# Kernel tuning notes

Hardware: AMD Instinct MI355X
Metric: run time of the kernel (lower is better)

## Reference

```python
import jax, jax.numpy as jnp
import numpy as np

S, D = 4096, 64
DROPOUT_P = 0.1


def setup_inputs() -> dict:
    key = jax.random.key(0)
    k1, k2, k3, k4, k5, k6 = jax.random.split(key, 6)
    return {
        "query": jax.random.normal(k1, (S, D), dtype=jnp.float32),
        "key": jax.random.normal(k2, (S, D), dtype=jnp.float32),
        "value": jax.random.normal(k3, (S, D), dtype=jnp.float32),
        "u_drop": jax.random.uniform(k4, (S, S), dtype=jnp.float32),
        "row_rand": jax.random.uniform(k5, (S, 1), dtype=jnp.float32),
        "x": jax.random.normal(k6, (1,), dtype=jnp.float32),
    }


def reference(query, key, value, u_drop, row_rand, x):
    d = query.shape[-1]
    # torch code divides by scale_factor = d**-0.5, i.e. multiplies by sqrt(d)
    qk = jnp.matmul(query, key.T) * jnp.asarray(d, query.dtype) ** 0.5  # [S,S]
    # dropout with keep prob (1-p), inverted scaling (matches F.dropout)
    keep = (u_drop >= DROPOUT_P).astype(qk.dtype) / (1.0 - DROPOUT_P)
    t = qk * keep  # [S,S]
    # drop_rows_or_cols: random floor mask normalized by its global sum
    r = jnp.floor(t * row_rand)          # [S,S] (row_rand broadcasts over cols)
    t = t * (r / jnp.sum(r))             # [S,S]
    return jnp.matmul(t, value)          # [S,D]
```

## Files before the change

### kernel.cpp

```cpp
#include <hip/hip_runtime.h>


#define S 4096
#define D 64
#define NCHUNK 16
#define JCHUNK (S / NCHUNK)
#define JT 64
#define NTILES (JCHUNK / JT)
#define KSCALE (8.0f / 0.9f)

typedef float f32x4 __attribute__((ext_vector_type(4)));
typedef short s16x8 __attribute__((ext_vector_type(8)));
typedef unsigned short u16x4 __attribute__((ext_vector_type(4)));
typedef int i32x4 __attribute__((ext_vector_type(4)));
typedef const __attribute__((address_space(1))) unsigned g_u32;
typedef __attribute__((address_space(3))) unsigned lds_u32;

__device__ inline unsigned short f2bf(float f) {
    union { float f; unsigned u; } v; v.f = f;
    unsigned r = v.u + 0x7fffu + ((v.u >> 16) & 1u);
    return (unsigned short)(r >> 16);
}

__device__ inline unsigned cvt_pk_bf16(float lo, float hi) {
    unsigned r;
    asm("v_cvt_pk_bf16_f32 %0, %1, %2" : "=v"(r) : "v"(lo), "v"(hi));
    return r;
}

__global__ void prep_all(const float* __restrict__ Kf,
                         const float* __restrict__ V,
                         short* __restrict__ Kbf,
                         short* __restrict__ VTbf,
                         int* __restrict__ sumr) {
    __shared__ short tile[64 * 68];
    const int b   = blockIdx.x;
    const int tid = threadIdx.x;
    if (b == 0 && tid == 0) *sumr = 0;

    if (b < 256) {
        const int k = b * 256 + tid;
        float4 v = ((const float4*)Kf)[k];
        u16x4 o; o[0] = f2bf(v.x * KSCALE); o[1] = f2bf(v.y * KSCALE);
                 o[2] = f2bf(v.z * KSCALE); o[3] = f2bf(v.w * KSCALE);
        ((u16x4*)Kbf)[k] = o;
    } else {
        const int j0 = (b - 256) * 64;
#pragma unroll
        for (int it = 0; it < 4; ++it) {
            const int f4 = tid + it * 256;
            const int row = f4 >> 4, c4 = (f4 & 15) * 4;
            float4 v = *(const float4*)&V[(size_t)(j0 + row) * D + c4];
            tile[(c4 + 0) * 68 + row] = (short)f2bf(v.x);
            tile[(c4 + 1) * 68 + row] = (short)f2bf(v.y);
            tile[(c4 + 2) * 68 + row] = (short)f2bf(v.z);
            tile[(c4 + 3) * 68 + row] = (short)f2bf(v.w);
        }
        __syncthreads();
#pragma unroll
        for (int it = 0; it < 4; ++it) {
            const int f4 = tid + it * 256;
            const int d = f4 >> 4, o4 = (f4 & 15) * 4;
            u16x4 w = *(const u16x4*)&tile[d * 68 + o4];
            *(u16x4*)&VTbf[(size_t)d * S + j0 + o4] = w;
        }
    }
}

__launch_bounds__(256, 4)
__global__ void fused_main(const float* __restrict__ Qf,
                           const short* __restrict__ Kbf,
                           const short* __restrict__ VTbf,
                           const float* __restrict__ Ud,
                           const float* __restrict__ RR,
                           float* __restrict__ Opart,
                           int* __restrict__ sumr)
{
    __shared__ short kb[2][8 * 512];
    __shared__ short vb[2][8 * 512];
    __shared__ int red[4];

    const int tid  = threadIdx.x;
    const int w    = tid >> 6;
    const int lane = tid & 63;
    const int quad = lane >> 4;
    const int n16  = lane & 15;

    const int ib  = blockIdx.x & 63;
    const int ic  = blockIdx.x >> 6;
    const int i0w = ib * 64 + w * 16;
    const int jbase = ic * JCHUNK;

    const float* uln = Ud + (size_t)(i0w + n16) * S + quad * 4;

    s16x8 aQ[2];
#pragma unroll
    for (int ks = 0; ks < 2; ++ks) {
        const float* qp = &Qf[(size_t)(i0w + n16) * D + ks * 32 + quad * 8];
        f32x4 qa = *(const f32x4*)qp;
        f32x4 qb = *(const f32x4*)(qp + 4);
        i32x4 aw;
        aw[0] = (int)cvt_pk_bf16(qa[0], qa[1]);
        aw[1] = (int)cvt_pk_bf16(qa[2], qa[3]);
        aw[2] = (int)cvt_pk_bf16(qb[0], qb[1]);
        aw[3] = (int)cvt_pk_bf16(qb[2], qb[3]);
        __builtin_memcpy(&aQ[ks], &aw, 16);
    }

    const float rrn = RR[i0w + n16];

    f32x4 accO[4];
#pragma unroll
    for (int ds = 0; ds < 4; ++ds) accO[ds] = (f32x4){0.f, 0.f, 0.f, 0.f};

    float lsum = 0.f;
    float4 un[4];
    unsigned um;

    {
#pragma unroll
        for (int p = 0; p < 2; ++p) {
            const int e = w * 2 + p;
            __builtin_amdgcn_global_load_lds(
                (g_u32*)&Kbf[(size_t)(jbase + (e >> 1) * 16 + n16) * D + (e & 1) * 32 + quad * 8],
                (lds_u32*)&kb[0][e * 512], 16, 0, 0);
        }
#pragma unroll
        for (int p = 0; p < 2; ++p) {
            const int e = w * 2 + p;
            __builtin_amdgcn_global_load_lds(
                (g_u32*)&VTbf[(size_t)((e & 3) * 16 + n16) * S + jbase + (e >> 2) * 32 + quad * 8],
                (lds_u32*)&vb[0][e * 512], 16, 0, 0);
        }
#pragma unroll
        for (int c = 0; c < 4; ++c)
            un[c] = *(const float4*)&uln[jbase + c * 16];
        __asm__ volatile("s_waitcnt vmcnt(4)" ::: "memory");
        __builtin_amdgcn_s_barrier();
        __asm__ volatile("" ::: "memory");
    }

#pragma unroll
    for (int jt = 0; jt < NTILES; ++jt) {
        const int bu = jt & 1;
        const int nb = bu ^ 1;
        const bool last = (jt + 1 == NTILES);

        if (!last) {
            const int j1 = jbase + (jt + 1) * JT;
#pragma unroll
            for (int p = 0; p < 2; ++p) {
                const int e = w * 2 + p;
                __builtin_amdgcn_global_load_lds(
                    (g_u32*)&Kbf[(size_t)(j1 + (e >> 1) * 16 + n16) * D + (e & 1) * 32 + quad * 8],
                    (lds_u32*)&kb[nb][e * 512], 16, 0, 0);
            }
#pragma unroll
            for (int p = 0; p < 2; ++p) {
                const int e = w * 2 + p;
                __builtin_amdgcn_global_load_lds(
                    (g_u32*)&VTbf[(size_t)((e & 3) * 16 + n16) * S + j1 + (e >> 2) * 32 + quad * 8],
                    (lds_u32*)&vb[nb][e * 512], 16, 0, 0);
            }
        }

        {
            unsigned m = 0;
#pragma unroll
            for (int c = 0; c < 4; ++c) {
                m |= (un[c].x >= 0.1f ? 1u : 0u) << (c * 4 + 0);
                m |= (un[c].y >= 0.1f ? 1u : 0u) << (c * 4 + 1);
                m |= (un[c].z >= 0.1f ? 1u : 0u) << (c * 4 + 2);
                m |= (un[c].w >= 0.1f ? 1u : 0u) << (c * 4 + 3);
            }
            um = m;
        }
        if (!last) {
            const int j1 = jbase + (jt + 1) * JT;
#pragma unroll
            for (int c = 0; c < 4; ++c)
                un[c] = *(const float4*)&uln[j1 + c * 16];
        }

        unsigned pkw[8];
#pragma unroll
        for (int cs = 0; cs < 4; ++cs) {
            f32x4 acc = (f32x4){0.f, 0.f, 0.f, 0.f};
#pragma unroll
            for (int ks = 0; ks < 2; ++ks) {
                s16x8 bK = *(const s16x8*)&kb[bu][(cs * 2 + ks) * 512 + lane * 8];
                acc = __builtin_amdgcn_mfma_f32_16x16x32_bf16(bK, aQ[ks], acc, 0, 0, 0);
            }
            float vv[4];
#pragma unroll
            for (int rg = 0; rg < 4; ++rg) {
                const float t = ((um >> (cs * 4 + rg)) & 1u) ? acc[rg] : 0.0f;
                const float r = floorf(t * rrn);
                lsum += r;
                vv[rg] = t * r;
            }
            pkw[cs * 2]     = cvt_pk_bf16(vv[0], vv[1]);
            pkw[cs * 2 + 1] = cvt_pk_bf16(vv[2], vv[3]);
        }

        const int pbase = (32 * ((lane >> 4) & 1) + n16) * 4;
#pragma unroll
        for (int ksj = 0; ksj < 2; ++ksj) {
            i32x4 aw;
#pragma unroll
            for (int widx = 0; widx < 4; ++widx) {
                const int addr = pbase + (widx >> 1) * 64;
                const int lo = __builtin_amdgcn_ds_bpermute(addr, (int)pkw[ksj * 4 + (widx & 1)]);
                const int hi = __builtin_amdgcn_ds_bpermute(addr, (int)pkw[ksj * 4 + 2 + (widx & 1)]);
                aw[widx] = (lane >= 32) ? hi : lo;
            }
            s16x8 aP;
            __builtin_memcpy(&aP, &aw, 16);
#pragma unroll
            for (int ds = 0; ds < 4; ++ds) {
                s16x8 bV = *(const s16x8*)&vb[bu][(ksj * 4 + ds) * 512 + lane * 8];
                accO[ds] = __builtin_amdgcn_mfma_f32_16x16x32_bf16(aP, bV, accO[ds], 0, 0, 0);
            }
        }

        if (!last) {
            __asm__ volatile("s_waitcnt vmcnt(4)" ::: "memory");
            __builtin_amdgcn_s_barrier();
            __asm__ volatile("" ::: "memory");
        }
    }

    float* op = Opart + (size_t)ic * S * D;
#pragma unroll
    for (int ds = 0; ds < 4; ++ds) {
        const int d = ds * 16 + n16;
#pragma unroll
        for (int rg = 0; rg < 4; ++rg) {
            const int i = i0w + quad * 4 + rg;
            op[(size_t)i * D + d] = accO[ds][rg];
        }
    }

    for (int off = 32; off; off >>= 1) lsum += __shfl_down(lsum, off);
    if (lane == 0) red[w] = (int)lsum;
    __syncthreads();
    if (tid == 0) atomicAdd(sumr, red[0] + red[1] + red[2] + red[3]);
}

__global__ void reduce_out(const float* __restrict__ Opart,
                           const int* __restrict__ sumr,
                           float* __restrict__ out) {
    const int idx = blockIdx.x * 256 + threadIdx.x;
    const float invR = 1.0f / (float)(*sumr);
    float sx = 0.f, sy = 0.f, sz = 0.f, sw = 0.f;
#pragma unroll
    for (int c = 0; c < NCHUNK; ++c) {
        const float4 v = ((const float4*)(Opart + (size_t)c * S * D))[idx];
        sx += v.x; sy += v.y; sz += v.z; sw += v.w;
    }
    float4 o; o.x = sx * invR; o.y = sy * invR; o.z = sz * invR; o.w = sw * invR;
    ((float4*)out)[idx] = o;
}

extern "C" void kernel_launch(void* const* d_in, const int* in_sizes, int n_in,
                              void* d_out, int out_size, void* d_ws, size_t ws_size,
                              hipStream_t stream) {
    (void)in_sizes; (void)n_in; (void)out_size; (void)ws_size;
    const float* Q  = (const float*)d_in[0];
    const float* Kf = (const float*)d_in[1];
    const float* V  = (const float*)d_in[2];
    const float* Ud = (const float*)d_in[3];
    const float* RR = (const float*)d_in[4];
    float* out = (float*)d_out;

    char* ws = (char*)d_ws;
    float* Opart = (float*)ws;
    short* Kbf  = (short*)(ws + (16u << 20));
    short* VTbf = (short*)(ws + (16u << 20) + (512u << 10));
    int*   sumr = (int*)  (ws + (16u << 20) + (1024u << 10));

    prep_all<<<dim3(320), dim3(256), 0, stream>>>(Kf, V, Kbf, VTbf, sumr);
    fused_main<<<dim3(64 * NCHUNK), dim3(256), 0, stream>>>(
        Q, Kbf, VTbf, Ud, RR, Opart, sumr);
    reduce_out<<<dim3(256), dim3(256), 0, stream>>>(Opart, sumr, out);
}
```

Before: 126.2 us.

## Split key dimension into more chunks and drop per-block tile loop

Doubles the number of key-dimension chunks so that each block handles one 128-column tile, loaded in a single shot. This replaces the previous 4-iteration double-buffered loop. The aim is to raise grid parallelism and cut the per-tile barrier and prefetch overhead. In exchange, the partial-output buffer doubles in size, which adds global writes in the main kernel and reads in the reduction kernel. The workspace layout is shifted to make room for it.

Result: slower. 133.0 us (+5.4%).

```diff
diff --git a/kernel.cpp b/kernel.cpp
--- a/kernel.cpp
+++ b/kernel.cpp
@@ -3,10 +3,8 @@
 
 #define S 4096
 #define D 64
-#define NCHUNK 16
-#define JCHUNK (S / NCHUNK)
-#define JT 64
-#define NTILES (JCHUNK / JT)
+#define NCHUNK 32
+#define JT 128
 #define KSCALE (8.0f / 0.9f)
 
 typedef float f32x4 __attribute__((ext_vector_type(4)));
@@ -76,8 +74,8 @@
                            float* __restrict__ Opart,
                            int* __restrict__ sumr)
 {
-    __shared__ short kb[2][8 * 512];
-    __shared__ short vb[2][8 * 512];
+    __shared__ short kb[16 * 512];
+    __shared__ short vb[16 * 512];
     __shared__ int red[4];
 
     const int tid  = threadIdx.x;
@@ -89,9 +87,28 @@
     const int ib  = blockIdx.x & 63;
     const int ic  = blockIdx.x >> 6;
     const int i0w = ib * 64 + w * 16;
-    const int jbase = ic * JCHUNK;
+    const int j0  = ic * JT;
 
     const float* uln = Ud + (size_t)(i0w + n16) * S + quad * 4;
+    float4 un[8];
+#pragma unroll
+    for (int c = 0; c < 8; ++c)
+        un[c] = *(const float4*)&uln[j0 + c * 16];
+
+#pragma unroll
+    for (int p = 0; p < 4; ++p) {
+        const int e = w * 4 + p;
+        __builtin_amdgcn_global_load_lds(
+            (g_u32*)&Kbf[(size_t)(j0 + (e >> 1) * 16 + n16) * D + (e & 1) * 32 + quad * 8],
+            (lds_u32*)&kb[e * 512], 16, 0, 0);
+    }
+#pragma unroll
+    for (int p = 0; p < 4; ++p) {
+        const int e = w * 4 + p;
+        __builtin_amdgcn_global_load_lds(
+            (g_u32*)&VTbf[(size_t)((e & 3) * 16 + n16) * S + j0 + (e >> 2) * 32 + quad * 8],
+            (lds_u32*)&vb[e * 512], 16, 0, 0);
+    }
 
     s16x8 aQ[2];
 #pragma unroll
@@ -106,127 +123,65 @@
         aw[3] = (int)cvt_pk_bf16(qb[2], qb[3]);
         __builtin_memcpy(&aQ[ks], &aw, 16);
     }
-
     const float rrn = RR[i0w + n16];
 
+    unsigned um = 0;
+#pragma unroll
+    for (int c = 0; c < 8; ++c) {
+        um |= (un[c].x >= 0.1f ? 1u : 0u) << (c * 4 + 0);
+        um |= (un[c].y >= 0.1f ? 1u : 0u) << (c * 4 + 1);
+        um |= (un[c].z >= 0.1f ? 1u : 0u) << (c * 4 + 2);
+        um |= (un[c].w >= 0.1f ? 1u : 0u) << (c * 4 + 3);
+    }
+
+    __asm__ volatile("s_waitcnt vmcnt(0)" ::: "memory");
+    __builtin_amdgcn_s_barrier();
+    __asm__ volatile("" ::: "memory");
+
+    float lsum = 0.f;
+
+    unsigned pkw[16];
+#pragma unroll
+    for (int cs = 0; cs < 8; ++cs) {
+        f32x4 acc = (f32x4){0.f, 0.f, 0.f, 0.f};
+#pragma unroll
+        for (int ks = 0; ks < 2; ++ks) {
+            s16x8 bK = *(const s16x8*)&kb[(cs * 2 + ks) * 512 + lane * 8];
+            acc = __builtin_amdgcn_mfma_f32_16x16x32_bf16(bK, aQ[ks], acc, 0, 0, 0);
+        }
+        float vv[4];
+#pragma unroll
+        for (int rg = 0; rg < 4; ++rg) {
+            const float t = ((um >> (cs * 4 + rg)) & 1u) ? acc[rg] : 0.0f;
+            const float r = floorf(t * rrn);
+            lsum += r;
+            vv[rg] = t * r;
+        }
+        pkw[cs * 2]     = cvt_pk_bf16(vv[0], vv[1]);
+        pkw[cs * 2 + 1] = cvt_pk_bf16(vv[2], vv[3]);
+    }
+
     f32x4 accO[4];
 #pragma unroll
     for (int ds = 0; ds < 4; ++ds) accO[ds] = (f32x4){0.f, 0.f, 0.f, 0.f};
 
-    float lsum = 0.f;
-    float4 un[4];
-    unsigned um;
-
-    {
-#pragma unroll
-        for (int p = 0; p < 2; ++p) {
-            const int e = w * 2 + p;
-            __builtin_amdgcn_global_load_lds(
-                (g_u32*)&Kbf[(size_t)(jbase + (e >> 1) * 16 + n16) * D + (e & 1) * 32 + quad * 8],
-                (lds_u32*)&kb[0][e * 512], 16, 0, 0);
-        }
-#pragma unroll
-        for (int p = 0; p < 2; ++p) {
-            const int e = w * 2 + p;
-            __builtin_amdgcn_global_load_lds(
-                (g_u32*)&VTbf[(size_t)((e & 3) * 16 + n16) * S + jbase + (e >> 2) * 32 + quad * 8],
-                (lds_u32*)&vb[0][e * 512], 16, 0, 0);
-        }
-#pragma unroll
-        for (int c = 0; c < 4; ++c)
-            un[c] = *(const float4*)&uln[jbase + c * 16];
-        __asm__ volatile("s_waitcnt vmcnt(4)" ::: "memory");
-        __builtin_amdgcn_s_barrier();
-        __asm__ volatile("" ::: "memory");
-    }
-
-#pragma unroll
-    for (int jt = 0; jt < NTILES; ++jt) {
-        const int bu = jt & 1;
-        const int nb = bu ^ 1;
-        const bool last = (jt + 1 == NTILES);
-
-        if (!last) {
-            const int j1 = jbase + (jt + 1) * JT;
-#pragma unroll
-            for (int p = 0; p < 2; ++p) {
-                const int e = w * 2 + p;
-                __builtin_amdgcn_global_load_lds(
-                    (g_u32*)&Kbf[(size_t)(j1 + (e >> 1) * 16 + n16) * D + (e & 1) * 32 + quad * 8],
-                    (lds_u32*)&kb[nb][e * 512], 16, 0, 0);
-            }
-#pragma unroll
-            for (int p = 0; p < 2; ++p) {
-                const int e = w * 2 + p;
-                __builtin_amdgcn_global_load_lds(
-                    (g_u32*)&VTbf[(size_t)((e & 3) * 16 + n16) * S + j1 + (e >> 2) * 32 + quad * 8],
-                    (lds_u32*)&vb[nb][e * 512], 16, 0, 0);
-            }
-        }
-
-        {
-            unsigned m = 0;
-#pragma unroll
-            for (int c = 0; c < 4; ++c) {
-                m |= (un[c].x >= 0.1f ? 1u : 0u) << (c * 4 + 0);
-                m |= (un[c].y >= 0.1f ? 1u : 0u) << (c * 4 + 1);
-                m |= (un[c].z >= 0.1f ? 1u : 0u) << (c * 4 + 2);
-                m |= (un[c].w >= 0.1f ? 1u : 0u) << (c * 4 + 3);
-            }
-            um = m;
-        }
-        if (!last) {
-            const int j1 = jbase + (jt + 1) * JT;
-#pragma unroll
-            for (int c = 0; c < 4; ++c)
-                un[c] = *(const float4*)&uln[j1 + c * 16];
-        }
-
-        unsigned pkw[8];
-#pragma unroll
-        for (int cs = 0; cs < 4; ++cs) {
-            f32x4 acc = (f32x4){0.f, 0.f, 0.f, 0.f};
-#pragma unroll
-            for (int ks = 0; ks < 2; ++ks) {
-                s16x8 bK = *(const s16x8*)&kb[bu][(cs * 2 + ks) * 512 + lane * 8];
-                acc = __builtin_amdgcn_mfma_f32_16x16x32_bf16(bK, aQ[ks], acc, 0, 0, 0);
-            }
-            float vv[4];
-#pragma unroll
-            for (int rg = 0; rg < 4; ++rg) {
-                const float t = ((um >> (cs * 4 + rg)) & 1u) ? acc[rg] : 0.0f;
-                const float r = floorf(t * rrn);
-                lsum += r;
-                vv[rg] = t * r;
-            }
-            pkw[cs * 2]     = cvt_pk_bf16(vv[0], vv[1]);
-            pkw[cs * 2 + 1] = cvt_pk_bf16(vv[2], vv[3]);
-        }
-
-        const int pbase = (32 * ((lane >> 4) & 1) + n16) * 4;
-#pragma unroll
-        for (int ksj = 0; ksj < 2; ++ksj) {
-            i32x4 aw;
-#pragma unroll
-            for (int widx = 0; widx < 4; ++widx) {
-                const int addr = pbase + (widx >> 1) * 64;
-                const int lo = __builtin_amdgcn_ds_bpermute(addr, (int)pkw[ksj * 4 + (widx & 1)]);
-                const int hi = __builtin_amdgcn_ds_bpermute(addr, (int)pkw[ksj * 4 + 2 + (widx & 1)]);
-                aw[widx] = (lane >= 32) ? hi : lo;
-            }
-            s16x8 aP;
-            __builtin_memcpy(&aP, &aw, 16);
-#pragma unroll
-            for (int ds = 0; ds < 4; ++ds) {
-                s16x8 bV = *(const s16x8*)&vb[bu][(ksj * 4 + ds) * 512 + lane * 8];
-                accO[ds] = __builtin_amdgcn_mfma_f32_16x16x32_bf16(aP, bV, accO[ds], 0, 0, 0);
-            }
-        }
-
-        if (!last) {
-            __asm__ volatile("s_waitcnt vmcnt(4)" ::: "memory");
-            __builtin_amdgcn_s_barrier();
-            __asm__ volatile("" ::: "memory");
+    const int pbase = (32 * ((lane >> 4) & 1) + n16) * 4;
+#pragma unroll
+    for (int ksj = 0; ksj < 4; ++ksj) {
+        i32x4 aw;
+#pragma unroll
+        for (int widx = 0; widx < 4; ++widx) {
+            const int addr = pbase + (widx >> 1) * 64;
+            const int lo = __builtin_amdgcn_ds_bpermute(addr, (int)pkw[ksj * 4 + (widx & 1)]);
+            const int hi = __builtin_amdgcn_ds_bpermute(addr, (int)pkw[ksj * 4 + 2 + (widx & 1)]);
+            aw[widx] = (lane >= 32) ? hi : lo;
+        }
+        s16x8 aP;
+        __builtin_memcpy(&aP, &aw, 16);
+#pragma unroll
+        for (int ds = 0; ds < 4; ++ds) {
+            s16x8 bV = *(const s16x8*)&vb[(ksj * 4 + ds) * 512 + lane * 8];
+            accO[ds] = __builtin_amdgcn_mfma_f32_16x16x32_bf16(aP, bV, accO[ds], 0, 0, 0);
         }
     }
 
@@ -275,9 +230,9 @@
 
     char* ws = (char*)d_ws;
     float* Opart = (float*)ws;
-    short* Kbf  = (short*)(ws + (16u << 20));
-    short* VTbf = (short*)(ws + (16u << 20) + (512u << 10));
-    int*   sumr = (int*)  (ws + (16u << 20) + (1024u << 10));
+    short* Kbf  = (short*)(ws + (32u << 20));
+    short* VTbf = (short*)(ws + (32u << 20) + (512u << 10));
+    int*   sumr = (int*)  (ws + (32u << 20) + (1024u << 10));
 
     prep_all<<<dim3(320), dim3(256), 0, stream>>>(Kf, V, Kbf, VTbf, sumr);
     fused_main<<<dim3(64 * NCHUNK), dim3(256), 0, stream>>>(
```
